# Performance work log

Measured on AMD Instinct MI355X. Metric: run time of the kernel, lower is better.

The kernel has to match this reference:

```python
import jax, jax.numpy as jnp
import numpy as np

# ---- static config (mirrors GptOssDecoderLayer init) ----
H = 1024      # hidden_size
HD = 64       # head_size
NQ = 16       # num_query_heads
NKV = 4       # num_key_value_heads
G = NQ // NKV # num_key_value_groups
E = 8         # num_experts
TOPK = 2      # experts_per_token
FFN = 1024    # expert intermediate (== hidden in GPT-OSS)
B, Q = 4, 128 # batch sequences, new query tokens per sequence
P, PS = 8, 128
S = P * PS    # kv length per sequence
T = B * Q     # total query tokens
SW = 128      # sliding window (layer_idx % 2 == 0 -> active)
LIMIT = 7.0   # swiglu_limit
ALPHA = 1.702
EPS = 1e-5
NEG = -1e30
SCALE = HD ** -0.5


def rmsnorm(x, w):
    return x * w * jax.lax.rsqrt(jnp.mean(x * x, axis=-1, keepdims=True) + EPS)


def setup_inputs() -> dict:
    key = jax.random.key(0)
    ks = jax.random.split(key, 16)
    hidden = jax.random.normal(ks[0], (T, H), jnp.float32)
    kv_cache = jax.random.normal(ks[1], (B * P, 2, PS, NKV, HD), jnp.float32)
    kv_page_indices = jnp.arange(B * P, dtype=jnp.int32).reshape(B, P)
    # additive causal mask: query q sits at absolute position S - Q + q
    qpos = S - Q + jnp.arange(Q)
    kpos = jnp.arange(S)
    causal = qpos[:, None] >= kpos[None, :]
    attention_mask = jnp.broadcast_to(
        jnp.where(causal, 0.0, NEG).astype(jnp.float32), (B, Q, S))
    sinks = 0.1 * jax.random.normal(ks[2], (NQ,), jnp.float32)
    w_qkv = jax.random.normal(ks[3], (H, HD * (NQ + 2 * NKV)), jnp.float32) / np.sqrt(H)
    b_qkv = jnp.zeros((HD * (NQ + 2 * NKV),), jnp.float32)
    w_o = jax.random.normal(ks[4], (NQ * HD, H), jnp.float32) / np.sqrt(NQ * HD)
    b_o = jnp.zeros((H,), jnp.float32)
    ln1_w = jnp.ones((H,), jnp.float32)
    ln2_w = jnp.ones((H,), jnp.float32)
    w_router = jax.random.normal(ks[5], (H, E), jnp.float32) / np.sqrt(H)
    b_router = jnp.zeros((E,), jnp.float32)
    w_gate_up = jax.random.normal(ks[6], (E, H, 2 * FFN), jnp.float32) / np.sqrt(H)
    b_gate_up = jnp.zeros((E, 2 * FFN), jnp.float32)
    w_down = jax.random.normal(ks[7], (E, FFN, H), jnp.float32) / np.sqrt(FFN)
    b_down = jnp.zeros((E, H), jnp.float32)
    return dict(hidden=hidden, kv_cache=kv_cache, attention_mask=attention_mask,
                kv_page_indices=kv_page_indices, sinks=sinks, w_qkv=w_qkv,
                b_qkv=b_qkv, w_o=w_o, b_o=b_o, ln1_w=ln1_w, ln2_w=ln2_w,
                w_router=w_router, b_router=b_router, w_gate_up=w_gate_up,
                b_gate_up=b_gate_up, w_down=w_down, b_down=b_down)


def reference(hidden, kv_cache, attention_mask, kv_page_indices, sinks,
              w_qkv, b_qkv, w_o, b_o, ln1_w, ln2_w, w_router, b_router,
              w_gate_up, b_gate_up, w_down, b_down):
    # ---- attention block ----
    x = rmsnorm(hidden, ln1_w)
    qkv = x @ w_qkv + b_qkv                       # [T, HD*(NQ+2*NKV)]
    q = qkv[:, :NQ * HD].reshape(B, Q, NQ, HD)
    k_new = qkv[:, NQ * HD:(NQ + NKV) * HD].reshape(B, Q, NKV, HD)
    v_new = qkv[:, (NQ + NKV) * HD:].reshape(B, Q, NKV, HD)
    # gather paged KV cache -> [B, S, NKV, HD]; write new tokens into tail slots
    pages = kv_cache[kv_page_indices]             # [B, P, 2, PS, NKV, HD]
    K = pages[:, :, 0].reshape(B, S, NKV, HD).at[:, S - Q:].set(k_new)
    V = pages[:, :, 1].reshape(B, S, NKV, HD).at[:, S - Q:].set(v_new)
    Kr = jnp.repeat(K, G, axis=2)                 # GQA expand -> [B, S, NQ, HD]
    Vr = jnp.repeat(V, G, axis=2)
    scores = jnp.einsum('bqhd,bshd->bhqs', q * SCALE, Kr) + attention_mask[:, None]
    # sliding-window (module trims pages outside the window; equivalent mask)
    qpos = S - Q + jnp.arange(Q)
    kpos = jnp.arange(S)
    win_ok = (qpos[:, None] - kpos[None, :]) < SW
    scores = jnp.where(win_ok[None, None], scores, NEG)
    m = jnp.max(scores, axis=-1)
    m = jnp.where(jnp.isinf(m) & (m < 0), 0.0, m)
    p = jnp.exp(scores - m[..., None])            # [B, NQ, Q, S]
    # attention sink joins the softmax denominator (online-softmax correction)
    denom = jnp.sum(p, axis=-1) + jnp.exp(sinks[None, :, None] - m)
    attn = jnp.einsum('bhqs,bshd->bhqd', p, Vr) / denom[..., None]
    attn = attn.transpose(0, 2, 1, 3).reshape(T, NQ * HD)
    h = hidden + attn @ w_o + b_o
    # ---- MoE block ----
    x2 = rmsnorm(h, ln2_w)
    logits = x2 @ w_router + b_router             # [T, E]
    vals, idx = jax.lax.top_k(logits, TOPK)
    wts = jax.nn.softmax(vals, axis=-1)
    comb = jnp.sum(jax.nn.one_hot(idx, E, dtype=x2.dtype) * wts[..., None], axis=1)
    gu = jnp.einsum('th,ehf->etf', x2, w_gate_up) + b_gate_up[:, None, :]
    gate = jnp.minimum(gu[..., 0::2], LIMIT)
    up = jnp.clip(gu[..., 1::2], -LIMIT, LIMIT)
    glu = gate * jax.nn.sigmoid(gate * ALPHA)
    eo = jnp.einsum('etf,efh->eth', (up + 1.0) * glu, w_down) + b_down[:, None, :]
    moe = jnp.einsum('te,eth->th', comb, eo)
    return h + moe
```

## Files before the change

### kernel.cpp

```cpp
#include <hip/hip_runtime.h>

constexpr int H    = 1024;
constexpr int HD   = 64;
constexpr int NQ   = 16;
constexpr int NKV  = 4;
constexpr int E_   = 8;
constexpr int FFN  = 1024;
constexpr int B_   = 4;
constexpr int Q_   = 128;
constexpr int P_   = 8;
constexpr int PS   = 128;
constexpr int S_   = P_ * PS;
constexpr int T_   = B_ * Q_;
constexpr int QKV_N = HD * (NQ + 2 * NKV);
constexpr float EPS   = 1e-5f;
constexpr float ALPHA = 1.702f;
constexpr float LIMIT = 7.0f;
constexpr float SCALE = 0.125f;

constexpr int MAXROWS = 1536;
constexpr int MAXTILES = 24;

typedef __attribute__((ext_vector_type(4))) float f32x4;
typedef __attribute__((ext_vector_type(8))) short s16x8;

__device__ __forceinline__ unsigned short f2bf(float f) {
    unsigned u = __float_as_uint(f);
    u += 0x7FFFu + ((u >> 16) & 1u);
    return (unsigned short)(u >> 16);
}

typedef __attribute__((address_space(3))) void lds_void;
typedef __attribute__((address_space(1))) void glb_void;
__device__ __forceinline__ void stage16(const void* g, void* l) {
    __builtin_amdgcn_global_load_lds((const glb_void*)g, (lds_void*)l, 16, 0, 0);
}

__device__ __forceinline__ void phase_barrier() {
    asm volatile("s_waitcnt vmcnt(0) lgkmcnt(0)" ::: "memory");
    __builtin_amdgcn_s_barrier();
}

#define COMPUTE(ABUF, WBUF)                                                                   \
    {                                                                                         \
        const char* Ab = (const char*)(ABUF);                                                 \
        s16x8 a0 = *(const s16x8*)(Ab + arow_off + aseg0 * 16);                               \
        s16x8 a1 = *(const s16x8*)(Ab + arow_off + aseg1 * 16);                               \
        const float* w0 = (const float*)(WBUF) + wbase0;                                      \
        const float* w1 = (const float*)(WBUF) + wbase1;                                      \
        float t0[8], t1[8], t2[8], t3[8];                                                     \
        _Pragma("unroll")                                                                     \
        for (int j = 0; j < 8; j++) {                                                         \
            t0[j] = w0[j * 32];        t1[j] = w1[j * 32];                                    \
            t2[j] = w0[1024 + j * 32]; t3[j] = w1[1024 + j * 32];                             \
        }                                                                                     \
        s16x8 b00, b01, b10, b11;                                                             \
        _Pragma("unroll")                                                                     \
        for (int j = 0; j < 8; j++) {                                                         \
            b00[j] = (short)f2bf(t0[j]); b01[j] = (short)f2bf(t1[j]);                         \
            b10[j] = (short)f2bf(t2[j]); b11[j] = (short)f2bf(t3[j]);                         \
        }                                                                                     \
        acc0 = __builtin_amdgcn_mfma_f32_16x16x32_bf16(a0, b00, acc0, 0, 0, 0);               \
        acc1 = __builtin_amdgcn_mfma_f32_16x16x32_bf16(a0, b01, acc1, 0, 0, 0);               \
        acc0 = __builtin_amdgcn_mfma_f32_16x16x32_bf16(a1, b10, acc0, 0, 0, 0);               \
        acc1 = __builtin_amdgcn_mfma_f32_16x16x32_bf16(a1, b11, acc1, 0, 0, 0);               \
    }

#define FRAG_SETUP                                                                            \
    int arow_off = (w * 16 + r16) * 128;                                                      \
    int aseg0 = kq ^ (r16 & 7);                                                               \
    int aseg1 = (kq | 4) ^ (r16 & 7);                                                         \
    int wsw = (kq & 1) << 4;                                                                  \
    int wbase0 = kq * 256 + (r16 ^ wsw);                                                      \
    int wbase1 = kq * 256 + ((16 + r16) ^ wsw);

__global__ __launch_bounds__(256) void rmsnorm_kernel(const float* __restrict__ in,
                                                      const float* __restrict__ w,
                                                      unsigned short* __restrict__ outb,
                                                      int* __restrict__ cnt) {
    int t   = blockIdx.x;
    int tid = threadIdx.x;
    if (t == 0 && tid < E_) cnt[tid] = 0;
    float4 v = ((const float4*)(in + (size_t)t * H))[tid];
    float ss = v.x * v.x + v.y * v.y + v.z * v.z + v.w * v.w;
#pragma unroll
    for (int off = 32; off; off >>= 1) ss += __shfl_down(ss, off);
    __shared__ float partial[4];
    __shared__ float s_inv;
    if ((tid & 63) == 0) partial[tid >> 6] = ss;
    __syncthreads();
    if (tid == 0)
        s_inv = rsqrtf((partial[0] + partial[1] + partial[2] + partial[3]) * (1.0f / H) + EPS);
    __syncthreads();
    float inv = s_inv;
    float4 wv = ((const float4*)w)[tid];
    ushort4 ob;
    ob.x = f2bf(v.x * wv.x * inv); ob.y = f2bf(v.y * wv.y * inv);
    ob.z = f2bf(v.z * wv.z * inv); ob.w = f2bf(v.w * wv.w * inv);
    ((ushort4*)(outb + (size_t)t * H))[tid] = ob;
}

__global__ __launch_bounds__(256) void gemm_dense_t(const unsigned short* __restrict__ Abf,
                                                    const float* __restrict__ W,
                                                    const float* __restrict__ bias,
                                                    const float* __restrict__ resid,
                                                    float* __restrict__ C,
                                                    float* __restrict__ Cdup, int N) {
    int nb = blockIdx.x, mb = blockIdx.y * 64;
    int tid = threadIdx.x;
    int w = tid >> 6, lane = tid & 63;
    int r16 = lane & 15, kq = lane >> 4;

    __shared__ __align__(16) char AfA[8192], AfB[8192], WfA[8192], WfB[8192];

    size_t sN = (size_t)N;
    int row0  = tid >> 3;
    int ss    = (tid & 7) ^ (row0 & 7);
    int wcol  = nb * 32 + (((tid & 7) * 4) ^ (((tid >> 6) & 1) << 4));
    int wvofs = (tid >> 6) * 1024;

    const unsigned short* pA0 = Abf + (size_t)(mb + row0) * 1024 + ss * 8;
    const unsigned short* pA1 = pA0 + 32 * 1024;

    FRAG_SETUP
    f32x4 acc0 = {}, acc1 = {};

    auto stageA = [&](char* dst, int T) {
        stage16(pA0 + T * 64, dst + wvofs);
        stage16(pA1 + T * 64, dst + wvofs + 4096);
    };
    auto stageW = [&](char* dst, int T) {
        stage16(W + (size_t)(T * 64 + row0) * sN + wcol, dst + wvofs);
        stage16(W + (size_t)(T * 64 + row0 + 32) * sN + wcol, dst + wvofs + 4096);
    };

    stageA(AfA, 0); stageW(WfA, 0);
    phase_barrier();
#pragma unroll
    for (int s = 0; s < 8; ++s) {
        stageA(AfB, 2 * s + 1); stageW(WfB, 2 * s + 1);
        __builtin_amdgcn_sched_barrier(0);
        COMPUTE(AfA, WfA)
        phase_barrier();
        if (2 * s + 2 < 16) {
            stageA(AfA, 2 * s + 2); stageW(WfA, 2 * s + 2);
            __builtin_amdgcn_sched_barrier(0);
        }
        COMPUTE(AfB, WfB)
        phase_barrier();
    }

    int row0e = mb + w * 16 + kq * 4;
    f32x4 accs[2] = {acc0, acc1};
#pragma unroll
    for (int nf = 0; nf < 2; nf++) {
        int col = nb * 32 + nf * 16 + r16;
        float bcol = bias[col];
#pragma unroll
        for (int r = 0; r < 4; r++) {
            int row = row0e + r;
            float v = accs[nf][r] + bcol;
            if (resid) v += resid[(size_t)row * sN + col];
            C[(size_t)row * sN + col] = v;
            if (Cdup) Cdup[(size_t)row * sN + col] = v;
        }
    }
}

__global__ __launch_bounds__(256) void attn_group_kernel(const float* __restrict__ qkv,
                                                         const float* __restrict__ kv_cache,
                                                         const int* __restrict__ page_idx,
                                                         const float* __restrict__ sinks,
                                                         unsigned short* __restrict__ attn_bf) {
    int blk = blockIdx.x;
    int kvh = blk & 3;
    int q   = (blk >> 2) & 127;
    int b   = blk >> 9;
    int t   = b * Q_ + q;
    int tid = threadIdx.x;
    int s_lo = S_ - Q_ - 127 + q;

    __shared__ __align__(16) float Vs[128][64];
    __shared__ __align__(16) float qs4[4][64];
    __shared__ float pv[4][128];
    __shared__ float sD[4];

#pragma unroll
    for (int r = 0; r < 8; r++) {
        int l = r * 256 + tid;
        int key = l >> 4, c = l & 15;
        int s = s_lo + key;
        const float* vp;
        if (s < S_ - Q_) {
            int page = page_idx[b * P_ + (s >> 7)];
            vp = kv_cache + (size_t)page * 65536 + 32768 + (size_t)(s & 127) * (NKV * HD) + kvh * HD;
        } else {
            vp = qkv + (size_t)(b * Q_ + (s - (S_ - Q_))) * QKV_N + (NQ + NKV) * HD + kvh * HD;
        }
        ((float4*)Vs[key])[c] = *(const float4*)(vp + c * 4);
    }
    {
        int hh = tid >> 6, d2 = tid & 63;
        qs4[hh][d2] = qkv[(size_t)t * QKV_N + (kvh * 4 + hh) * HD + d2];
    }
    __syncthreads();

    {
        int key = tid & 127, hp = tid >> 7;
        int s = s_lo + key;
        const float* kp;
        if (s < S_ - Q_) {
            int page = page_idx[b * P_ + (s >> 7)];
            kp = kv_cache + (size_t)page * 65536 + (size_t)(s & 127) * (NKV * HD) + kvh * HD;
        } else {
            kp = qkv + (size_t)(b * Q_ + (s - (S_ - Q_))) * QKV_N + NQ * HD + kvh * HD;
        }
        const float4* kp4 = (const float4*)kp;
        const float4* q0p = (const float4*)qs4[hp * 2];
        const float4* q1p = (const float4*)qs4[hp * 2 + 1];
        float sc0 = 0.f, sc1 = 0.f;
#pragma unroll
        for (int d4 = 0; d4 < 16; d4++) {
            float4 kk = kp4[d4];
            float4 q0 = q0p[d4], q1 = q1p[d4];
            sc0 += q0.x * kk.x + q0.y * kk.y + q0.z * kk.z + q0.w * kk.w;
            sc1 += q1.x * kk.x + q1.y * kk.y + q1.z * kk.z + q1.w * kk.w;
        }
        pv[hp * 2][key]     = sc0 * SCALE;
        pv[hp * 2 + 1][key] = sc1 * SCALE;
    }
    __syncthreads();

    {
        int wv = tid >> 6, lane = tid & 63;
        float a0 = pv[wv][lane], a1 = pv[wv][lane + 64];
        float m = fmaxf(a0, a1);
#pragma unroll
        for (int off = 32; off; off >>= 1) m = fmaxf(m, __shfl_xor(m, off));
        float p0 = __expf(a0 - m), p1 = __expf(a1 - m);
        float l = p0 + p1;
#pragma unroll
        for (int off = 32; off; off >>= 1) l += __shfl_xor(l, off);
        pv[wv][lane] = p0;
        pv[wv][lane + 64] = p1;
        if (lane == 0) sD[wv] = l + __expf(sinks[kvh * 4 + wv] - m);
    }
    __syncthreads();

    {
        int hh = tid >> 6, d2 = tid & 63;
        float a0 = 0.f, a1 = 0.f, a2 = 0.f, a3 = 0.f;
#pragma unroll 4
        for (int i = 0; i < 128; i += 4) {
            a0 += pv[hh][i]     * Vs[i][d2];
            a1 += pv[hh][i + 1] * Vs[i + 1][d2];
            a2 += pv[hh][i + 2] * Vs[i + 2][d2];
            a3 += pv[hh][i + 3] * Vs[i + 3][d2];
        }
        float acc = ((a0 + a1) + (a2 + a3)) / sD[hh];
        attn_bf[(size_t)t * (NQ * HD) + (kvh * 4 + hh) * HD + d2] = f2bf(acc);
    }
}

__global__ __launch_bounds__(256) void rms_router_kernel(const float* __restrict__ hbuf,
                                                         const float* __restrict__ ln2w,
                                                         const float* __restrict__ w_router,
                                                         const float* __restrict__ b_router,
                                                         unsigned short* __restrict__ x2bf,
                                                         int* __restrict__ ridx,
                                                         float* __restrict__ rwt,
                                                         int* __restrict__ cnt) {
    int t = blockIdx.x;
    int tid = threadIdx.x;
    float4 v = ((const float4*)(hbuf + (size_t)t * H))[tid];
    float ss = v.x * v.x + v.y * v.y + v.z * v.z + v.w * v.w;
#pragma unroll
    for (int off = 32; off; off >>= 1) ss += __shfl_down(ss, off);
    __shared__ float partial[4];
    __shared__ float s_inv;
    if ((tid & 63) == 0) partial[tid >> 6] = ss;
    __syncthreads();
    if (tid == 0)
        s_inv = rsqrtf((partial[0] + partial[1] + partial[2] + partial[3]) * (1.0f / H) + EPS);
    __syncthreads();
    float inv = s_inv;
    float4 wv = ((const float4*)ln2w)[tid];
    float4 o;
    o.x = v.x * wv.x * inv; o.y = v.y * wv.y * inv;
    o.z = v.z * wv.z * inv; o.w = v.w * wv.w * inv;
    ushort4 ob;
    ob.x = f2bf(o.x); ob.y = f2bf(o.y); ob.z = f2bf(o.z); ob.w = f2bf(o.w);
    ((ushort4*)(x2bf + (size_t)t * H))[tid] = ob;

    const float4* wr = (const float4*)(w_router + (size_t)tid * 4 * E_);
    float p[E_];
    {
        float4 r0a = wr[0], r0b = wr[1];
        float4 r1a = wr[2], r1b = wr[3];
        float4 r2a = wr[4], r2b = wr[5];
        float4 r3a = wr[6], r3b = wr[7];
        p[0] = o.x * r0a.x + o.y * r1a.x + o.z * r2a.x + o.w * r3a.x;
        p[1] = o.x * r0a.y + o.y * r1a.y + o.z * r2a.y + o.w * r3a.y;
        p[2] = o.x * r0a.z + o.y * r1a.z + o.z * r2a.z + o.w * r3a.z;
        p[3] = o.x * r0a.w + o.y * r1a.w + o.z * r2a.w + o.w * r3a.w;
        p[4] = o.x * r0b.x + o.y * r1b.x + o.z * r2b.x + o.w * r3b.x;
        p[5] = o.x * r0b.y + o.y * r1b.y + o.z * r2b.y + o.w * r3b.y;
        p[6] = o.x * r0b.z + o.y * r1b.z + o.z * r2b.z + o.w * r3b.z;
        p[7] = o.x * r0b.w + o.y * r1b.w + o.z * r2b.w + o.w * r3b.w;
    }
    __shared__ float wsum[4][E_];
    int wv2 = tid >> 6, lane = tid & 63;
#pragma unroll
    for (int e = 0; e < E_; e++) {
        float r = p[e];
#pragma unroll
        for (int off = 32; off; off >>= 1) r += __shfl_xor(r, off);
        if (lane == 0) wsum[wv2][e] = r;
    }
    __syncthreads();
    __shared__ float logits[E_];
    if (tid < E_)
        logits[tid] = wsum[0][tid] + wsum[1][tid] + wsum[2][tid] + wsum[3][tid] + b_router[tid];
    __syncthreads();
    if (tid == 0) {
        int i0 = 0; float v0 = logits[0];
        for (int ee = 1; ee < E_; ee++)
            if (logits[ee] > v0) { v0 = logits[ee]; i0 = ee; }
        int i1 = -1; float v1 = -3.4e38f;
        for (int ee = 0; ee < E_; ee++)
            if (ee != i0 && logits[ee] > v1) { v1 = logits[ee]; i1 = ee; }
        float w0 = 1.0f / (1.0f + __expf(v1 - v0));
        ridx[t * 2] = i0; ridx[t * 2 + 1] = i1;
        rwt[t * 2] = w0;  rwt[t * 2 + 1] = 1.0f - w0;
        atomicAdd(&cnt[i0], 1);
        atomicAdd(&cnt[i1], 1);
    }
}

__global__ __launch_bounds__(256) void plumb_kernel(const int* __restrict__ cnt,
                                                    const int* __restrict__ ridx,
                                                    int* __restrict__ poff,
                                                    int* __restrict__ list,
                                                    int* __restrict__ tmap) {
    __shared__ int lpos[E_], lpoff[E_];
    int tid = threadIdx.x;
    if (tid == 0) {
        int run = 0, it = 0;
        for (int e = 0; e < E_; e++) {
            lpoff[e] = run; poff[e] = run;
            int pc = (cnt[e] + 63) & ~63;
            for (int tl = 0; tl < (pc >> 6); tl++) tmap[1 + it++] = (e << 5) | tl;
            run += pc;
        }
        tmap[0] = it;
    }
    if (tid < E_) lpos[tid] = 0;
    __syncthreads();
    for (int i = tid; i < 2 * T_; i += 256) {
        int e = ridx[i];
        int pp = atomicAdd(&lpos[e], 1);
        list[lpoff[e] + pp] = i;
    }
}

__global__ __launch_bounds__(256) void moe_gateup_t(const unsigned short* __restrict__ x2bf,
                                                    const int* __restrict__ list,
                                                    const int* __restrict__ cnt,
                                                    const int* __restrict__ poff,
                                                    const int* __restrict__ tmap,
                                                    const float* __restrict__ wgu,
                                                    const float* __restrict__ bgu,
                                                    unsigned short* __restrict__ act_bf) {
    if ((int)blockIdx.y >= tmap[0]) return;
    int v0m = tmap[1 + blockIdx.y];
    int e = v0m >> 5, tl = v0m & 31;
    int n = cnt[e];
    int base = poff[e];
    int nb = blockIdx.x;
    int tid = threadIdx.x;
    int w = tid >> 6, lane = tid & 63;
    int r16 = lane & 15, kq = lane >> 4;

    __shared__ __align__(16) char AfA[8192], AfB[8192], WfA[8192], WfB[8192];

    int row0  = tid >> 3;
    int ss    = (tid & 7) ^ (row0 & 7);
    int wcol  = nb * 32 + (((tid & 7) * 4) ^ (((tid >> 6) & 1) << 4));
    int wvofs = (tid >> 6) * 1024;

    const float* Wg = wgu + (size_t)e * (1024 * 2048);
    int rr0 = tl * 64 + row0;
    int rr1 = rr0 + 32;
    int tok0 = (rr0 < n) ? list[base + rr0] : list[base];
    int tok1 = (rr1 < n) ? list[base + rr1] : list[base];
    const unsigned short* pA0 = x2bf + (size_t)(tok0 >> 1) * 1024 + ss * 8;
    const unsigned short* pA1 = x2bf + (size_t)(tok1 >> 1) * 1024 + ss * 8;

    FRAG_SETUP
    f32x4 acc0 = {}, acc1 = {};

    auto stageA = [&](char* dst, int T) {
        stage16(pA0 + T * 64, dst + wvofs);
        stage16(pA1 + T * 64, dst + wvofs + 4096);
    };
    auto stageW = [&](char* dst, int T) {
        stage16(Wg + (size_t)(T * 64 + row0) * 2048 + wcol, dst + wvofs);
        stage16(Wg + (size_t)(T * 64 + row0 + 32) * 2048 + wcol, dst + wvofs + 4096);
    };

    stageA(AfA, 0); stageW(WfA, 0);
    phase_barrier();
#pragma unroll
    for (int s = 0; s < 8; ++s) {
        stageA(AfB, 2 * s + 1); stageW(WfB, 2 * s + 1);
        __builtin_amdgcn_sched_barrier(0);
        COMPUTE(AfA, WfA)
        phase_barrier();
        if (2 * s + 2 < 16) {
            stageA(AfA, 2 * s + 2); stageW(WfA, 2 * s + 2);
            __builtin_amdgcn_sched_barrier(0);
        }
        COMPUTE(AfB, WfB)
        phase_barrier();
    }

    int parity = r16 & 1;
    f32x4 accs[2] = {acc0, acc1};
#pragma unroll
    for (int nf = 0; nf < 2; nf++) {
        int gucol = nb * 32 + nf * 16 + r16;
        float bb = bgu[(size_t)e * 2048 + gucol];
#pragma unroll
        for (int r = 0; r < 4; r++) {
            float v = accs[nf][r] + bb;
            float o = __shfl_xor(v, 1);
            if (!parity) {
                float g = fminf(v, LIMIT);
                float u = fminf(fmaxf(o, -LIMIT), LIMIT);
                float glu = g / (1.0f + __expf(-ALPHA * g));
                int rr = tl * 64 + w * 16 + kq * 4 + r;
                if (rr < n)
                    act_bf[(size_t)(base + rr) * FFN + (gucol >> 1)] = f2bf((u + 1.0f) * glu);
            }
        }
    }
}

__global__ __launch_bounds__(256) void moe_down_t(const unsigned short* __restrict__ act_bf,
                                                  const int* __restrict__ list,
                                                  const int* __restrict__ cnt,
                                                  const int* __restrict__ poff,
                                                  const int* __restrict__ tmap,
                                                  const float* __restrict__ rwt,
                                                  const float* __restrict__ wdn,
                                                  const float* __restrict__ b_down,
                                                  float* __restrict__ out) {
    if ((int)blockIdx.y >= tmap[0]) return;
    int v0m = tmap[1 + blockIdx.y];
    int e = v0m >> 5, tl = v0m & 31;
    int n = cnt[e];
    int base = poff[e];
    int nb = blockIdx.x;
    int z  = blockIdx.z;
    int tid = threadIdx.x;
    int w = tid >> 6, lane = tid & 63;
    int r16 = lane & 15, kq = lane >> 4;

    __shared__ __align__(16) char AfA[8192], AfB[8192], WfA[8192], WfB[8192];

    int row0  = tid >> 3;
    int ss    = (tid & 7) ^ (row0 & 7);
    int wcol  = nb * 32 + (((tid & 7) * 4) ^ (((tid >> 6) & 1) << 4));
    int wvofs = (tid >> 6) * 1024;

    const float* Wg = wdn + (size_t)e * (1024 * 1024) + (size_t)(z * 512) * 1024;
    const unsigned short* pA0 = act_bf + (size_t)(base + tl * 64 + row0) * 1024 + z * 512 + ss * 8;
    const unsigned short* pA1 = pA0 + 32 * 1024;

    FRAG_SETUP
    f32x4 acc0 = {}, acc1 = {};

    auto stageA = [&](char* dst, int T) {
        stage16(pA0 + T * 64, dst + wvofs);
        stage16(pA1 + T * 64, dst + wvofs + 4096);
    };
    auto stageW = [&](char* dst, int T) {
        stage16(Wg + (size_t)(T * 64 + row0) * 1024 + wcol, dst + wvofs);
        stage16(Wg + (size_t)(T * 64 + row0 + 32) * 1024 + wcol, dst + wvofs + 4096);
    };

    stageA(AfA, 0); stageW(WfA, 0);
    phase_barrier();
#pragma unroll
    for (int s = 0; s < 4; ++s) {
        stageA(AfB, 2 * s + 1); stageW(WfB, 2 * s + 1);
        __builtin_amdgcn_sched_barrier(0);
        COMPUTE(AfA, WfA)
        phase_barrier();
        if (2 * s + 2 < 8) {
            stageA(AfA, 2 * s + 2); stageW(WfA, 2 * s + 2);
            __builtin_amdgcn_sched_barrier(0);
        }
        COMPUTE(AfB, WfB)
        phase_barrier();
    }

    f32x4 accs[2] = {acc0, acc1};
#pragma unroll
    for (int r = 0; r < 4; r++) {
        int rr = tl * 64 + w * 16 + kq * 4 + r;
        if (rr < n) {
            int t2 = list[base + rr];
            float sc = rwt[t2];
            float* op = out + (size_t)(t2 >> 1) * H;
#pragma unroll
            for (int nf = 0; nf < 2; nf++) {
                int col = nb * 32 + nf * 16 + r16;
                float v = accs[nf][r] + (z == 0 ? b_down[(size_t)e * 1024 + col] : 0.0f);
                atomicAdd(op + col, sc * v);
            }
        }
    }
}

extern "C" void kernel_launch(void* const* d_in, const int* in_sizes, int n_in,
                              void* d_out, int out_size, void* d_ws, size_t ws_size,
                              hipStream_t stream) {
    const float* hidden          = (const float*)d_in[0];
    const float* kv_cache        = (const float*)d_in[1];
    const int*   kv_page_indices = (const int*)d_in[3];
    const float* sinks           = (const float*)d_in[4];
    const float* w_qkv           = (const float*)d_in[5];
    const float* b_qkv           = (const float*)d_in[6];
    const float* w_o             = (const float*)d_in[7];
    const float* b_o             = (const float*)d_in[8];
    const float* ln1_w           = (const float*)d_in[9];
    const float* ln2_w           = (const float*)d_in[10];
    const float* w_router        = (const float*)d_in[11];
    const float* b_router        = (const float*)d_in[12];
    const float* w_gate_up       = (const float*)d_in[13];
    const float* b_gate_up       = (const float*)d_in[14];
    const float* w_down          = (const float*)d_in[15];
    const float* b_down          = (const float*)d_in[16];
    float* out = (float*)d_out;

    char* base = (char*)d_ws;
    float* qkv   = (float*)base;                       base += (size_t)T_ * QKV_N * 4;
    float* hbuf  = (float*)base;                       base += (size_t)T_ * H * 4;
    unsigned short* x_bf    = (unsigned short*)base;   base += (size_t)T_ * H * 2;
    unsigned short* x2_bf   = (unsigned short*)base;   base += (size_t)T_ * H * 2;
    unsigned short* attn_bf = (unsigned short*)base;   base += (size_t)T_ * NQ * HD * 2;
    unsigned short* act_bf  = (unsigned short*)base;   base += (size_t)(MAXROWS + 128) * FFN * 2;
    float* rwt  = (float*)base;                        base += 2 * T_ * 4;
    int*   ridx = (int*)base;                          base += 2 * T_ * 4;
    int*   cnt  = (int*)base;                          base += E_ * 4;
    int*   poff = (int*)base;                          base += E_ * 4;
    int*   list = (int*)base;                          base += MAXROWS * 4;
    int*   tmap = (int*)base;                          base += (1 + MAXTILES + 7) * 4;

    rmsnorm_kernel<<<T_, 256, 0, stream>>>(hidden, ln1_w, x_bf, cnt);
    gemm_dense_t<<<dim3(QKV_N / 32, T_ / 64), 256, 0, stream>>>(
        x_bf, w_qkv, b_qkv, nullptr, qkv, nullptr, QKV_N);
    attn_group_kernel<<<B_ * Q_ * NKV, 256, 0, stream>>>(qkv, kv_cache, kv_page_indices, sinks, attn_bf);
    gemm_dense_t<<<dim3(H / 32, T_ / 64), 256, 0, stream>>>(
        attn_bf, w_o, b_o, hidden, hbuf, out, H);
    rms_router_kernel<<<T_, 256, 0, stream>>>(hbuf, ln2_w, w_router, b_router,
                                              x2_bf, ridx, rwt, cnt);
    plumb_kernel<<<1, 256, 0, stream>>>(cnt, ridx, poff, list, tmap);
    moe_gateup_t<<<dim3(FFN * 2 / 32, MAXTILES), 256, 0, stream>>>(
        x2_bf, list, cnt, poff, tmap, w_gate_up, b_gate_up, act_bf);
    moe_down_t<<<dim3(H / 32, MAXTILES, 2), 256, 0, stream>>>(
        act_bf, list, cnt, poff, tmap, rwt, w_down, b_down, out);
}
```

Baseline: 285.0 us.

## Enlarge MoE expert GEMM row tiles to 128 and remap blocks for weight reuse

Expert tiles grow from 64 to 128 token rows. Each wave now computes a 32x32 output using four MFMA accumulators, so every fp32 weight tile loaded and converted to bf16 serves twice as many rows. This cuts weight traffic and conversion work per row. The grid is flattened to 1D, with block ids swizzled so consecutive blocks share a column slice across tiles, which is meant to improve L2 reuse of weights. In exchange, padding to 128 rows wastes more work on sparsely used experts, the LDS footprint doubles, and register pressure rises.

```diff
diff --git a/kernel.cpp b/kernel.cpp
--- a/kernel.cpp
+++ b/kernel.cpp
@@ -18,8 +18,8 @@
 constexpr float LIMIT = 7.0f;
 constexpr float SCALE = 0.125f;
 
-constexpr int MAXROWS = 1536;
-constexpr int MAXTILES = 24;
+constexpr int MAXROWS  = 2048;
+constexpr int MAXTILES = 16;
 
 typedef __attribute__((ext_vector_type(4))) float f32x4;
 typedef __attribute__((ext_vector_type(8))) short s16x8;
@@ -40,6 +40,14 @@
     asm volatile("s_waitcnt vmcnt(0) lgkmcnt(0)" ::: "memory");
     __builtin_amdgcn_s_barrier();
 }
+
+#define FRAG_SETUP                                                                            \
+    int arow_off = (w * 16 + r16) * 128;                                                      \
+    int aseg0 = kq ^ (r16 & 7);                                                               \
+    int aseg1 = (kq | 4) ^ (r16 & 7);                                                         \
+    int wsw = (kq & 1) << 4;                                                                  \
+    int wbase0 = kq * 256 + (r16 ^ wsw);                                                      \
+    int wbase1 = kq * 256 + ((16 + r16) ^ wsw);
 
 #define COMPUTE(ABUF, WBUF)                                                                   \
     {                                                                                         \
@@ -66,13 +74,45 @@
         acc1 = __builtin_amdgcn_mfma_f32_16x16x32_bf16(a1, b11, acc1, 0, 0, 0);               \
     }
 
-#define FRAG_SETUP                                                                            \
-    int arow_off = (w * 16 + r16) * 128;                                                      \
+#define FRAG_SETUP2                                                                           \
+    int arow0 = (w * 32 + r16) * 128;                                                         \
+    int arow1 = arow0 + 16 * 128;                                                             \
     int aseg0 = kq ^ (r16 & 7);                                                               \
     int aseg1 = (kq | 4) ^ (r16 & 7);                                                         \
     int wsw = (kq & 1) << 4;                                                                  \
     int wbase0 = kq * 256 + (r16 ^ wsw);                                                      \
     int wbase1 = kq * 256 + ((16 + r16) ^ wsw);
+
+#define COMPUTE2(ABUF, WBUF)                                                                  \
+    {                                                                                         \
+        const char* Ab = (const char*)(ABUF);                                                 \
+        s16x8 a00 = *(const s16x8*)(Ab + arow0 + aseg0 * 16);                                 \
+        s16x8 a01 = *(const s16x8*)(Ab + arow0 + aseg1 * 16);                                 \
+        s16x8 a10 = *(const s16x8*)(Ab + arow1 + aseg0 * 16);                                 \
+        s16x8 a11 = *(const s16x8*)(Ab + arow1 + aseg1 * 16);                                 \
+        const float* w0 = (const float*)(WBUF) + wbase0;                                      \
+        const float* w1 = (const float*)(WBUF) + wbase1;                                      \
+        float t0[8], t1[8], t2[8], t3[8];                                                     \
+        _Pragma("unroll")                                                                     \
+        for (int j = 0; j < 8; j++) {                                                         \
+            t0[j] = w0[j * 32];        t1[j] = w1[j * 32];                                    \
+            t2[j] = w0[1024 + j * 32]; t3[j] = w1[1024 + j * 32];                             \
+        }                                                                                     \
+        s16x8 b00, b01, b10, b11;                                                             \
+        _Pragma("unroll")                                                                     \
+        for (int j = 0; j < 8; j++) {                                                         \
+            b00[j] = (short)f2bf(t0[j]); b01[j] = (short)f2bf(t1[j]);                         \
+            b10[j] = (short)f2bf(t2[j]); b11[j] = (short)f2bf(t3[j]);                         \
+        }                                                                                     \
+        acc00 = __builtin_amdgcn_mfma_f32_16x16x32_bf16(a00, b00, acc00, 0, 0, 0);            \
+        acc01 = __builtin_amdgcn_mfma_f32_16x16x32_bf16(a00, b01, acc01, 0, 0, 0);            \
+        acc10 = __builtin_amdgcn_mfma_f32_16x16x32_bf16(a10, b00, acc10, 0, 0, 0);            \
+        acc11 = __builtin_amdgcn_mfma_f32_16x16x32_bf16(a10, b01, acc11, 0, 0, 0);            \
+        acc00 = __builtin_amdgcn_mfma_f32_16x16x32_bf16(a01, b10, acc00, 0, 0, 0);            \
+        acc01 = __builtin_amdgcn_mfma_f32_16x16x32_bf16(a01, b11, acc01, 0, 0, 0);            \
+        acc10 = __builtin_amdgcn_mfma_f32_16x16x32_bf16(a11, b10, acc10, 0, 0, 0);            \
+        acc11 = __builtin_amdgcn_mfma_f32_16x16x32_bf16(a11, b11, acc11, 0, 0, 0);            \
+    }
 
 __global__ __launch_bounds__(256) void rmsnorm_kernel(const float* __restrict__ in,
                                                       const float* __restrict__ w,
@@ -348,8 +388,8 @@
         int run = 0, it = 0;
         for (int e = 0; e < E_; e++) {
             lpoff[e] = run; poff[e] = run;
-            int pc = (cnt[e] + 63) & ~63;
-            for (int tl = 0; tl < (pc >> 6); tl++) tmap[1 + it++] = (e << 5) | tl;
+            int pc = (cnt[e] + 127) & ~127;
+            for (int tl = 0; tl < (pc >> 7); tl++) tmap[1 + it++] = (e << 5) | tl;
             run += pc;
         }
         tmap[0] = it;
@@ -371,41 +411,57 @@
                                                     const float* __restrict__ wgu,
                                                     const float* __restrict__ bgu,
                                                     unsigned short* __restrict__ act_bf) {
-    if ((int)blockIdx.y >= tmap[0]) return;
-    int v0m = tmap[1 + blockIdx.y];
+    int bid = blockIdx.x;
+    int ti = (bid >> 9) * 8 + (bid & 7);
+    if (ti >= tmap[0]) return;
+    int nb = (bid >> 3) & 63;
+    int v0m = tmap[1 + ti];
     int e = v0m >> 5, tl = v0m & 31;
     int n = cnt[e];
     int base = poff[e];
-    int nb = blockIdx.x;
     int tid = threadIdx.x;
     int w = tid >> 6, lane = tid & 63;
     int r16 = lane & 15, kq = lane >> 4;
 
-    __shared__ __align__(16) char AfA[8192], AfB[8192], WfA[8192], WfB[8192];
-
-    int row0  = tid >> 3;
-    int ss    = (tid & 7) ^ (row0 & 7);
+    __shared__ __align__(16) char AfA[16384], AfB[16384], WfA[8192], WfB[8192];
+
+    int rlo   = (tid >> 3) & 7;
+    int ss    = (tid & 7) ^ rlo;
+    int rbase = (tid >> 6) * 32 + rlo;
+    int wrow  = tid >> 3;
     int wcol  = nb * 32 + (((tid & 7) * 4) ^ (((tid >> 6) & 1) << 4));
-    int wvofs = (tid >> 6) * 1024;
+    int wv4096 = (tid >> 6) * 4096;
+    int wv1024 = (tid >> 6) * 1024;
 
     const float* Wg = wgu + (size_t)e * (1024 * 2048);
-    int rr0 = tl * 64 + row0;
-    int rr1 = rr0 + 32;
-    int tok0 = (rr0 < n) ? list[base + rr0] : list[base];
-    int tok1 = (rr1 < n) ? list[base + rr1] : list[base];
-    const unsigned short* pA0 = x2bf + (size_t)(tok0 >> 1) * 1024 + ss * 8;
-    const unsigned short* pA1 = x2bf + (size_t)(tok1 >> 1) * 1024 + ss * 8;
-
-    FRAG_SETUP
-    f32x4 acc0 = {}, acc1 = {};
+    const unsigned short* pA0;
+    const unsigned short* pA1;
+    const unsigned short* pA2;
+    const unsigned short* pA3;
+    {
+        int r0c = tl * 128 + rbase;
+        int k0 = (r0c      < n) ? list[base + r0c]      : list[base];
+        int k1 = (r0c + 8  < n) ? list[base + r0c + 8]  : list[base];
+        int k2 = (r0c + 16 < n) ? list[base + r0c + 16] : list[base];
+        int k3 = (r0c + 24 < n) ? list[base + r0c + 24] : list[base];
+        pA0 = x2bf + (size_t)(k0 >> 1) * 1024 + ss * 8;
+        pA1 = x2bf + (size_t)(k1 >> 1) * 1024 + ss * 8;
+        pA2 = x2bf + (size_t)(k2 >> 1) * 1024 + ss * 8;
+        pA3 = x2bf + (size_t)(k3 >> 1) * 1024 + ss * 8;
+    }
+
+    FRAG_SETUP2
+    f32x4 acc00 = {}, acc01 = {}, acc10 = {}, acc11 = {};
 
     auto stageA = [&](char* dst, int T) {
-        stage16(pA0 + T * 64, dst + wvofs);
-        stage16(pA1 + T * 64, dst + wvofs + 4096);
+        stage16(pA0 + T * 64, dst + wv4096);
+        stage16(pA1 + T * 64, dst + wv4096 + 1024);
+        stage16(pA2 + T * 64, dst + wv4096 + 2048);
+        stage16(pA3 + T * 64, dst + wv4096 + 3072);
     };
     auto stageW = [&](char* dst, int T) {
-        stage16(Wg + (size_t)(T * 64 + row0) * 2048 + wcol, dst + wvofs);
-        stage16(Wg + (size_t)(T * 64 + row0 + 32) * 2048 + wcol, dst + wvofs + 4096);
+        stage16(Wg + (size_t)(T * 64 + wrow) * 2048 + wcol, dst + wv1024);
+        stage16(Wg + (size_t)(T * 64 + wrow + 32) * 2048 + wcol, dst + wv1024 + 4096);
     };
 
     stageA(AfA, 0); stageW(WfA, 0);
@@ -414,36 +470,38 @@
     for (int s = 0; s < 8; ++s) {
         stageA(AfB, 2 * s + 1); stageW(WfB, 2 * s + 1);
         __builtin_amdgcn_sched_barrier(0);
-        COMPUTE(AfA, WfA)
+        COMPUTE2(AfA, WfA)
         phase_barrier();
         if (2 * s + 2 < 16) {
             stageA(AfA, 2 * s + 2); stageW(WfA, 2 * s + 2);
             __builtin_amdgcn_sched_barrier(0);
         }
-        COMPUTE(AfB, WfB)
+        COMPUTE2(AfB, WfB)
         phase_barrier();
     }
 
     int parity = r16 & 1;
-    f32x4 accs[2] = {acc0, acc1};
-#pragma unroll
-    for (int nf = 0; nf < 2; nf++) {
-        int gucol = nb * 32 + nf * 16 + r16;
-        float bb = bgu[(size_t)e * 2048 + gucol];
-#pragma unroll
-        for (int r = 0; r < 4; r++) {
-            float v = accs[nf][r] + bb;
-            float o = __shfl_xor(v, 1);
-            if (!parity) {
-                float g = fminf(v, LIMIT);
-                float u = fminf(fmaxf(o, -LIMIT), LIMIT);
-                float glu = g / (1.0f + __expf(-ALPHA * g));
-                int rr = tl * 64 + w * 16 + kq * 4 + r;
-                if (rr < n)
-                    act_bf[(size_t)(base + rr) * FFN + (gucol >> 1)] = f2bf((u + 1.0f) * glu);
+    f32x4 am[2][2] = {{acc00, acc01}, {acc10, acc11}};
+#pragma unroll
+    for (int mf = 0; mf < 2; mf++)
+#pragma unroll
+        for (int nf = 0; nf < 2; nf++) {
+            int gucol = nb * 32 + nf * 16 + r16;
+            float bb = bgu[(size_t)e * 2048 + gucol];
+#pragma unroll
+            for (int r = 0; r < 4; r++) {
+                float v = am[mf][nf][r] + bb;
+                float o = __shfl_xor(v, 1);
+                if (!parity) {
+                    float g = fminf(v, LIMIT);
+                    float u = fminf(fmaxf(o, -LIMIT), LIMIT);
+                    float glu = g / (1.0f + __expf(-ALPHA * g));
+                    int rr = tl * 128 + w * 32 + mf * 16 + kq * 4 + r;
+                    if (rr < n)
+                        act_bf[(size_t)(base + rr) * FFN + (gucol >> 1)] = f2bf((u + 1.0f) * glu);
+                }
             }
         }
-    }
 }
 
 __global__ __launch_bounds__(256) void moe_down_t(const unsigned short* __restrict__ act_bf,
@@ -455,38 +513,47 @@
                                                   const float* __restrict__ wdn,
                                                   const float* __restrict__ b_down,
                                                   float* __restrict__ out) {
-    if ((int)blockIdx.y >= tmap[0]) return;
-    int v0m = tmap[1 + blockIdx.y];
+    int bid = blockIdx.x;
+    int u = (bid >> 8) * 8 + (bid & 7);
+    int ti = u >> 1, z = u & 1;
+    if (ti >= tmap[0]) return;
+    int nb = (bid >> 3) & 31;
+    int v0m = tmap[1 + ti];
     int e = v0m >> 5, tl = v0m & 31;
     int n = cnt[e];
     int base = poff[e];
-    int nb = blockIdx.x;
-    int z  = blockIdx.z;
     int tid = threadIdx.x;
     int w = tid >> 6, lane = tid & 63;
     int r16 = lane & 15, kq = lane >> 4;
 
-    __shared__ __align__(16) char AfA[8192], AfB[8192], WfA[8192], WfB[8192];
-
-    int row0  = tid >> 3;
-    int ss    = (tid & 7) ^ (row0 & 7);
+    __shared__ __align__(16) char AfA[16384], AfB[16384], WfA[8192], WfB[8192];
+
+    int rlo   = (tid >> 3) & 7;
+    int ss    = (tid & 7) ^ rlo;
+    int rbase = (tid >> 6) * 32 + rlo;
+    int wrow  = tid >> 3;
     int wcol  = nb * 32 + (((tid & 7) * 4) ^ (((tid >> 6) & 1) << 4));
-    int wvofs = (tid >> 6) * 1024;
+    int wv4096 = (tid >> 6) * 4096;
+    int wv1024 = (tid >> 6) * 1024;
 
     const float* Wg = wdn + (size_t)e * (1024 * 1024) + (size_t)(z * 512) * 1024;
-    const unsigned short* pA0 = act_bf + (size_t)(base + tl * 64 + row0) * 1024 + z * 512 + ss * 8;
-    const unsigned short* pA1 = pA0 + 32 * 1024;
-
-    FRAG_SETUP
-    f32x4 acc0 = {}, acc1 = {};
+    const unsigned short* pA0 = act_bf + (size_t)(base + tl * 128 + rbase) * 1024 + z * 512 + ss * 8;
+    const unsigned short* pA1 = pA0 + (size_t)8 * 1024;
+    const unsigned short* pA2 = pA0 + (size_t)16 * 1024;
+    const unsigned short* pA3 = pA0 + (size_t)24 * 1024;
+
+    FRAG_SETUP2
+    f32x4 acc00 = {}, acc01 = {}, acc10 = {}, acc11 = {};
 
     auto stageA = [&](char* dst, int T) {
-        stage16(pA0 + T * 64, dst + wvofs);
-        stage16(pA1 + T * 64, dst + wvofs + 4096);
+        stage16(pA0 + T * 64, dst + wv4096);
+        stage16(pA1 + T * 64, dst + wv4096 + 1024);
+        stage16(pA2 + T * 64, dst + wv4096 + 2048);
+        stage16(pA3 + T * 64, dst + wv4096 + 3072);
     };
     auto stageW = [&](char* dst, int T) {
-        stage16(Wg + (size_t)(T * 64 + row0) * 1024 + wcol, dst + wvofs);
-        stage16(Wg + (size_t)(T * 64 + row0 + 32) * 1024 + wcol, dst + wvofs + 4096);
+        stage16(Wg + (size_t)(T * 64 + wrow) * 1024 + wcol, dst + wv1024);
+        stage16(Wg + (size_t)(T * 64 + wrow + 32) * 1024 + wcol, dst + wv1024 + 4096);
     };
 
     stageA(AfA, 0); stageW(WfA, 0);
@@ -495,32 +562,34 @@
     for (int s = 0; s < 4; ++s) {
         stageA(AfB, 2 * s + 1); stageW(WfB, 2 * s + 1);
         __builtin_amdgcn_sched_barrier(0);
-        COMPUTE(AfA, WfA)
+        COMPUTE2(AfA, WfA)
         phase_barrier();
         if (2 * s + 2 < 8) {
             stageA(AfA, 2 * s + 2); stageW(WfA, 2 * s + 2);
             __builtin_amdgcn_sched_barrier(0);
         }
-        COMPUTE(AfB, WfB)
+        COMPUTE2(AfB, WfB)
         phase_barrier();
     }
 
-    f32x4 accs[2] = {acc0, acc1};
-#pragma unroll
-    for (int r = 0; r < 4; r++) {
-        int rr = tl * 64 + w * 16 + kq * 4 + r;
-        if (rr < n) {
-            int t2 = list[base + rr];
-            float sc = rwt[t2];
-            float* op = out + (size_t)(t2 >> 1) * H;
-#pragma unroll
-            for (int nf = 0; nf < 2; nf++) {
-                int col = nb * 32 + nf * 16 + r16;
-                float v = accs[nf][r] + (z == 0 ? b_down[(size_t)e * 1024 + col] : 0.0f);
-                atomicAdd(op + col, sc * v);
+    f32x4 am[2][2] = {{acc00, acc01}, {acc10, acc11}};
+#pragma unroll
+    for (int mf = 0; mf < 2; mf++)
+#pragma unroll
+        for (int r = 0; r < 4; r++) {
+            int rr = tl * 128 + w * 32 + mf * 16 + kq * 4 + r;
+            if (rr < n) {
+                int t2 = list[base + rr];
+                float sc = rwt[t2];
+                float* op = out + (size_t)(t2 >> 1) * H;
+#pragma unroll
+                for (int nf = 0; nf < 2; nf++) {
+                    int col = nb * 32 + nf * 16 + r16;
+                    float v = am[mf][nf][r] + (z == 0 ? b_down[(size_t)e * 1024 + col] : 0.0f);
+                    atomicAdd(op + col, sc * v);
+                }
             }
         }
-    }
 }
 
 extern "C" void kernel_launch(void* const* d_in, const int* in_sizes, int n_in,
@@ -567,8 +636,8 @@
     rms_router_kernel<<<T_, 256, 0, stream>>>(hbuf, ln2_w, w_router, b_router,
                                               x2_bf, ridx, rwt, cnt);
     plumb_kernel<<<1, 256, 0, stream>>>(cnt, ridx, poff, list, tmap);
-    moe_gateup_t<<<dim3(FFN * 2 / 32, MAXTILES), 256, 0, stream>>>(
+    moe_gateup_t<<<64 * MAXTILES, 256, 0, stream>>>(
         x2_bf, list, cnt, poff, tmap, w_gate_up, b_gate_up, act_bf);
-    moe_down_t<<<dim3(H / 32, MAXTILES, 2), 256, 0, stream>>>(
+    moe_down_t<<<32 * MAXTILES * 2, 256, 0, stream>>>(
         act_bf, list, cnt, poff, tmap, rwt, w_down, b_down, out);
 }
```

After: 288.9 us. About the same (+1.3%).
